# Optimization experiments

Measured on AMD Instinct MI355X. Metric: run time of the kernel, lower is better.

Reference implementation:

```python
import jax, jax.numpy as jnp
import numpy as np

B, T, N, E = 8, 64, 32, 256          # batch, seq_len, subgraph nodes, subgraph edges
D, H = 512, 8                        # embed dim, GAT heads (head dim D//H)
NV = 60000                           # total graph nodes (rows of X)
LS, LG = 10000, 60000                # last_idx_senses, last_idx_globals
V = LG - LS                          # globals vocab = 50000
DH = D // H
H1 = D                               # h1 state dim (include_senses=False)
CI = 2 * D                           # concatenated input dim


def setup_inputs() -> dict:
    key = jax.random.key(0)
    ks = jax.random.split(key, 32)
    s = 0.02
    inp = {
        "x_indices": jax.random.randint(ks[0], (B, T, N), 0, NV),
        "edge_index": jax.random.randint(ks[1], (B, T, 2, E), 0, N),
        "X": jax.random.normal(ks[2], (NV, D), jnp.float32) * s,
        "W_gat": jax.random.normal(ks[3], (D, D), jnp.float32) * s,
        "att_src": jax.random.normal(ks[4], (H, DH), jnp.float32) * s,
        "att_dst": jax.random.normal(ks[5], (H, DH), jnp.float32) * s,
        "b_gat": jnp.zeros((D,), jnp.float32),
        "Wz1": jax.random.normal(ks[6], (CI, H1), jnp.float32) * s,
        "Uz1": jax.random.normal(ks[7], (H1, H1), jnp.float32) * s,
        "Wr1": jax.random.normal(ks[8], (CI, H1), jnp.float32) * s,
        "Ur1": jax.random.normal(ks[9], (H1, H1), jnp.float32) * s,
        "W1": jax.random.normal(ks[10], (CI, H1), jnp.float32) * s,
        "bW1": jnp.zeros((H1,), jnp.float32),
        "U1": jax.random.normal(ks[11], (H1, H1), jnp.float32) * s,
        "bU1": jnp.zeros((H1,), jnp.float32),
        "Wz2": jax.random.normal(ks[12], (H1, D), jnp.float32) * s,
        "Uz2": jax.random.normal(ks[13], (D, D), jnp.float32) * s,
        "Wr2": jax.random.normal(ks[14], (H1, D), jnp.float32) * s,
        "Ur2": jax.random.normal(ks[15], (D, D), jnp.float32) * s,
        "W2": jax.random.normal(ks[16], (H1, D), jnp.float32) * s,
        "bW2": jnp.zeros((D,), jnp.float32),
        "U2": jax.random.normal(ks[17], (D, D), jnp.float32) * s,
        "bU2": jnp.zeros((D,), jnp.float32),
        "Wg": jax.random.normal(ks[18], (D, V), jnp.float32) * s,
        "bg": jnp.zeros((V,), jnp.float32),
    }
    return inp


def _gat(x, src, dst, W_gat, att_src, att_dst, b_gat):
    # x: [N,D]; src/dst: [E+N] (self-loops appended). PyG GATConv, concat heads.
    xW = (x @ W_gat).reshape(N, H, DH)                     # [N,H,DH]
    a_s = jnp.einsum('nhd,hd->nh', xW, att_src)
    a_d = jnp.einsum('nhd,hd->nh', xW, att_dst)
    e = jax.nn.leaky_relu(a_s[src] + a_d[dst], 0.2)        # [Etot,H]
    m = jax.ops.segment_max(e, dst, num_segments=N)
    m = jnp.where(jnp.isfinite(m), m, 0.0)
    ex = jnp.exp(e - m[dst])
    den = jax.ops.segment_sum(ex, dst, num_segments=N)
    alpha = ex / (den[dst] + 1e-16)                        # softmax per target node
    out = jax.ops.segment_sum(alpha[:, :, None] * xW[src], dst, num_segments=N)
    return out.reshape(N, D) + b_gat


def reference(x_indices, edge_index, X, W_gat, att_src, att_dst, b_gat,
              Wz1, Uz1, Wr1, Ur1, W1, bW1, U1, bU1,
              Wz2, Uz2, Wr2, Ur2, W2, bW2, U2, bU2, Wg, bg):
    S = B * T
    idx = x_indices.reshape(S, N)
    ei = edge_index.reshape(S, 2, E)
    loops = jnp.broadcast_to(jnp.arange(N), (S, N))
    src = jnp.concatenate([ei[:, 0], loops], axis=1)       # [S, E+N]
    dst = jnp.concatenate([ei[:, 1], loops], axis=1)

    x_nodes = X[idx]                                       # [S,N,D] gather
    gat = jax.vmap(lambda xs, s_, d_: _gat(xs, s_, d_, W_gat, att_src, att_dst, b_gat))
    gat_out = gat(x_nodes, src, dst)                       # [S,N,D]

    # input_signals = [current word embedding, GAT state of node 0]
    inp = jnp.concatenate([x_nodes[:, 0, :], gat_out[:, 0, :]], axis=1)  # [S,2D]

    def step(carry, u):
        h1, h2 = carry
        z1 = jax.nn.sigmoid(u @ Wz1 + h1 @ Uz1)
        r1 = jax.nn.sigmoid(u @ Wr1 + h1 @ Ur1)
        ht1 = jnp.tanh(u @ W1 + bW1 + (r1 * h1) @ U1 + bU1)
        h1n = z1 * ht1 + (1.0 - z1) * h1
        z2 = jax.nn.sigmoid(h1n @ Wz2 + h2 @ Uz2)
        r2 = jax.nn.sigmoid(h1n @ Wr2 + h2 @ Ur2)
        ht2 = jnp.tanh(h1n @ W2 + bW2 + (r2 * h2) @ U2 + bU2)
        h2n = z2 * ht2 + (1.0 - z2) * h2
        # torch code overwrites memory via .data.copy_ -> recurrence is detached
        new_carry = (jax.lax.stop_gradient(h1n), jax.lax.stop_gradient(h2n))
        return new_carry, h2n

    carry0 = (jnp.zeros((H1,), inp.dtype), jnp.zeros((D,), inp.dtype))
    _, H2 = jax.lax.scan(step, carry0, inp)                # [S,D]

    logits = H2 @ Wg + bg                                  # [S,V]
    return jax.nn.log_softmax(logits, axis=-1)
```

## Files before the change

### kernel.cpp

```cpp
#include <hip/hip_runtime.h>


typedef unsigned short u16;
typedef unsigned long long u64;
typedef __attribute__((ext_vector_type(8))) short s16x8;
typedef __attribute__((ext_vector_type(8))) u16  u16x8;
typedef __attribute__((ext_vector_type(4))) float f32x4;

__device__ __forceinline__ float bf2f(u16 u) {
    unsigned int x = ((unsigned int)u) << 16;
    return __uint_as_float(x);
}
__device__ __forceinline__ u16 f2bf(float f) {
    unsigned int x = __float_as_uint(f);
    x = x + 0x7fffu + ((x >> 16) & 1u);
    return (u16)(x >> 16);
}
__device__ __forceinline__ float sigmoidf_(float x) { return 1.f / (1.f + __expf(-x)); }
__device__ __forceinline__ float ldin(const void* p, size_t i, int m) {
    return m ? ((const float*)p)[i] : bf2f(((const u16*)p)[i]);
}
__device__ __forceinline__ bool nanf_(float v) { return !(v == v); }

__device__ __forceinline__ u64 packtag(float v, unsigned int e) {
    return ((u64)e << 32) | (u64)__float_as_uint(v);
}
__device__ __forceinline__ float tagval(u64 x) { return __uint_as_float((unsigned int)x); }
__device__ __forceinline__ unsigned int tagof(u64 x) { return (unsigned int)(x >> 32); }

#define AL64(p) __hip_atomic_load((p), __ATOMIC_RELAXED, __HIP_MEMORY_SCOPE_AGENT)
#define AS64(p, v) __hip_atomic_store((p), (v), __ATOMIC_RELAXED, __HIP_MEMORY_SCOPE_AGENT)

#define S_SEQ 512
#define NND   32
#define DIM   512
#define NHEAD 8
#define CI    1024
#define NV3   1536
#define VOC   50000
#define KWG   64
#define TSTEPS 512

#define OFF_MODE    0
#define OFF_FLAGS   4
#define OFF_ROWSUM  256
#define OFF_G1      4096
#define OFF_G2      12288
#define OFF_R1      20480
#define OFF_R2      24576
#define ZERO_BYTES  28672
#define OFF_WAS     28672
#define OFF_WAD     45056
#define OFF_INP     61440
#define OFF_A1      1110016
#define OFF_H2      4255744
#define OFF_WST     4780032
#define OFF_WCATT   9498624
#define OFF_WGT     12644352
#define WGT_BYTES   (50048ull * 512ull * 2ull)
#define WS_NEED_BIG (12644352ull + WGT_BYTES)

__global__ void detect_mode(const void* X, int* mode) {
    const u16* p = (const u16*)X;
    int tid = threadIdx.x;
    int hits = 0;
    for (int i = tid; i < 1024; i += 64) {
        u16 u = p[i];
        if ((u & 0x7f80u) >= 0x4000u) hits++;
    }
    hits += __shfl_xor(hits, 1);  hits += __shfl_xor(hits, 2);
    hits += __shfl_xor(hits, 4);  hits += __shfl_xor(hits, 8);
    hits += __shfl_xor(hits, 16); hits += __shfl_xor(hits, 32);
    if (tid == 0) *mode = (hits > 8) ? 1 : 0;
}

__global__ void prep_att(const void* __restrict__ Wgat, const void* __restrict__ asrc,
                         const void* __restrict__ adst, float* __restrict__ WAs,
                         float* __restrict__ WAd, const int* __restrict__ modep) {
    const int m = *modep;
    int id = blockIdx.x * 256 + threadIdx.x;
    int which = id >> 12;
    int rem = id & 4095;
    int d = rem >> 3, h = rem & 7;
    const void* att = which ? adst : asrc;
    float sum = 0.f;
#pragma unroll 8
    for (int k = 0; k < 64; ++k)
        sum += ldin(Wgat, d * 512 + h * 64 + k, m) * ldin(att, h * 64 + k, m);
    (which ? WAd : WAs)[d * 8 + h] = sum;
}

struct Ptrs9 { const void* p[9]; };
__global__ void transpose9(Ptrs9 ps, u16* __restrict__ dst, const int* __restrict__ modep) {
    const int m = *modep;
    __shared__ u16 tile[32][33];
    const void* src = ps.p[blockIdx.z];
    u16* d = dst + (size_t)blockIdx.z * 262144;
    int c0 = blockIdx.x * 32, r0 = blockIdx.y * 32;
    int tx = threadIdx.x & 31, ty = threadIdx.x >> 5;
#pragma unroll
    for (int i = 0; i < 32; i += 8)
        tile[ty + i][tx] = f2bf(ldin(src, (size_t)(r0 + ty + i) * 512 + c0 + tx, m));
    __syncthreads();
#pragma unroll
    for (int i = 0; i < 32; i += 8)
        d[(size_t)(c0 + ty + i) * 512 + r0 + tx] = tile[tx][ty + i];
}

struct Ptrs3 { const void* p[3]; };
__global__ void transpose3(Ptrs3 ps, u16* __restrict__ dst, const int* __restrict__ modep) {
    const int m = *modep;
    __shared__ u16 tile[32][33];
    const void* src = ps.p[blockIdx.z];
    u16* d = dst + (size_t)blockIdx.z * 524288;
    int c0 = blockIdx.x * 32, r0 = blockIdx.y * 32;
    int tx = threadIdx.x & 31, ty = threadIdx.x >> 5;
#pragma unroll
    for (int i = 0; i < 32; i += 8)
        tile[ty + i][tx] = f2bf(ldin(src, (size_t)(r0 + ty + i) * 512 + c0 + tx, m));
    __syncthreads();
#pragma unroll
    for (int i = 0; i < 32; i += 8)
        d[(size_t)(c0 + ty + i) * 1024 + r0 + tx] = tile[tx][ty + i];
}

__global__ void transpose_wg(const void* __restrict__ Wg, u16* __restrict__ dst,
                             const int* __restrict__ modep) {
    const int m = *modep;
    __shared__ u16 tile[32][33];
    int c0 = blockIdx.x * 32;
    int r0 = blockIdx.y * 32;
    int tx = threadIdx.x & 31, ty = threadIdx.x >> 5;
#pragma unroll
    for (int i = 0; i < 32; i += 8) {
        int n = c0 + tx;
        tile[ty + i][tx] = (n < VOC)
            ? f2bf(ldin(Wg, (size_t)(r0 + ty + i) * VOC + n, m)) : (u16)0;
    }
    __syncthreads();
#pragma unroll
    for (int i = 0; i < 32; i += 8) {
        int n = c0 + ty + i;
        if (n < VOC) dst[(size_t)n * 512 + r0 + tx] = tile[tx][ty + i];
    }
}

__global__ __launch_bounds__(256) void gat_kernel(
    const int* __restrict__ xidx, const int* __restrict__ eidx,
    const void* __restrict__ X, const void* __restrict__ Wgat,
    const float* __restrict__ WAs, const float* __restrict__ WAd,
    const void* __restrict__ bgat, u16* __restrict__ inp,
    const int* __restrict__ modep, int* __restrict__ flags) {
    const int m = *modep;
    int s = blockIdx.x, tid = threadIdx.x;
    __shared__ int idxL[NND];
    __shared__ int srcL[260];
    __shared__ int nsrcL;
    __shared__ float asL[NND][NHEAD];
    __shared__ float ad0[NHEAD];
    __shared__ float scoresL[257 * NHEAD];
    __shared__ float denL[NHEAD];
    __shared__ float xbL[NHEAD][DIM];

    if (tid < NND) idxL[tid] = xidx[s * NND + tid];
    if (tid == 0) nsrcL = 0;
    __syncthreads();

    {
        int n = tid >> 3, h = tid & 7;
        size_t xoff = (size_t)idxL[n] * DIM;
        float acc = 0.f, accd = 0.f;
        for (int d = 0; d < DIM; ++d) {
            float xv = ldin(X, xoff + d, m);
            acc  += xv * WAs[d * 8 + h];
            accd += xv * WAd[d * 8 + h];
        }
        asL[n][h] = acc;
        if (n == 0) ad0[h] = accd;
    }
    {
        int dstn = eidx[s * 512 + 256 + tid];
        if (dstn == 0) {
            int p = atomicAdd(&nsrcL, 1);
            srcL[p] = eidx[s * 512 + tid];
        }
        if (tid == 0) { int p = atomicAdd(&nsrcL, 1); srcL[p] = 0; }
    }
    __syncthreads();
    int nsrc = nsrcL;

    for (int p = tid; p < nsrc * NHEAD; p += 256) {
        int le = p >> 3, h = p & 7;
        float e = asL[srcL[le]][h] + ad0[h];
        e = (e >= 0.f) ? e : 0.2f * e;
        scoresL[le * 8 + h] = e;
    }
    __syncthreads();
    if (tid < NHEAD) {
        int h = tid;
        float mx = -1e30f;
        for (int le = 0; le < nsrc; ++le) mx = fmaxf(mx, scoresL[le * 8 + h]);
        float den = 0.f;
        for (int le = 0; le < nsrc; ++le) {
            float ex = __expf(scoresL[le * 8 + h] - mx);
            scoresL[le * 8 + h] = ex;
            den += ex;
        }
        denL[h] = den + 1e-16f;
    }
    __syncthreads();
    for (int p = tid; p < NHEAD * DIM; p += 256) {
        int d = p & 511, h = p >> 9;
        float acc = 0.f;
        for (int le = 0; le < nsrc; ++le)
            acc += scoresL[le * 8 + h] * ldin(X, (size_t)idxL[srcL[le]] * DIM + d, m);
        xbL[h][d] = acc / denL[h];
    }
    __syncthreads();
    for (int c = tid; c < DIM; c += 256) {
        int h = c >> 6;
        float acc = 0.f;
        for (int d = 0; d < DIM; ++d)
            acc += xbL[h][d] * ldin(Wgat, d * 512 + c, m);
        acc += ldin(bgat, c, m);
        float xv = ldin(X, (size_t)idxL[0] * DIM + c, m);
        if (nanf_(acc)) { atomicOr(flags, 1); acc = 0.f; }
        if (nanf_(xv))  { atomicOr(flags, 1); xv  = 0.f; }
        inp[(size_t)s * CI + DIM + c] = f2bf(acc);
        inp[(size_t)s * CI + c] = f2bf(xv);
    }
}

__global__ __launch_bounds__(256) void gemm_a1(
    const u16* __restrict__ A, const u16* __restrict__ BT,
    const void* __restrict__ bW1, const void* __restrict__ bU1,
    float* __restrict__ C, const int* __restrict__ modep, int* __restrict__ flags) {
    const int m = *modep;
    const int K = CI;
    int tid = threadIdx.x, wave = tid >> 6, lane = tid & 63;
    int mw = wave & 1, nw = wave >> 1, l15 = lane & 15, q = lane >> 4;
    int mbase = blockIdx.y * 64 + mw * 32;
    int nbase = blockIdx.x * 128 + nw * 64;
    f32x4 acc[2][4];
#pragma unroll
    for (int mi = 0; mi < 2; ++mi)
#pragma unroll
        for (int ni = 0; ni < 4; ++ni) acc[mi][ni] = (f32x4){0.f, 0.f, 0.f, 0.f};
    for (int k0 = 0; k0 < K; k0 += 32) {
        s16x8 a[2], b[4];
#pragma unroll
        for (int mi = 0; mi < 2; ++mi)
            a[mi] = *(const s16x8*)(A + (size_t)(mbase + mi * 16 + l15) * K + k0 + q * 8);
#pragma unroll
        for (int ni = 0; ni < 4; ++ni)
            b[ni] = *(const s16x8*)(BT + (size_t)(nbase + ni * 16 + l15) * K + k0 + q * 8);
#pragma unroll
        for (int mi = 0; mi < 2; ++mi)
#pragma unroll
            for (int ni = 0; ni < 4; ++ni)
                acc[mi][ni] = __builtin_amdgcn_mfma_f32_16x16x32_bf16(a[mi], b[ni], acc[mi][ni], 0, 0, 0);
    }
#pragma unroll
    for (int mi = 0; mi < 2; ++mi)
#pragma unroll
        for (int r = 0; r < 4; ++r) {
            int row = mbase + mi * 16 + q * 4 + r;
#pragma unroll
            for (int ni = 0; ni < 4; ++ni) {
                int col = nbase + ni * 16 + l15;
                float v = acc[mi][ni][r];
                if (col >= 1024) v += ldin(bW1, col - 1024, m) + ldin(bU1, col - 1024, m);
                if (nanf_(v)) { atomicOr(flags, 2); v = 0.f; }
                C[(size_t)row * NV3 + col] = v;
            }
        }
}

__global__ __launch_bounds__(256) void scan_kernel(
    const float* __restrict__ A1, const u16* __restrict__ wsT,
    const void* __restrict__ bW2, const void* __restrict__ bU2,
    u64* __restrict__ h1x, u64* __restrict__ h2x,
    u64* __restrict__ r1x, u64* __restrict__ r2x,
    u16* __restrict__ H2,
    const int* __restrict__ modep, int* __restrict__ flags) {
    const int m_ = *modep;
    const int wg = blockIdx.x;
    const int tid = threadIdx.x;
    const int jj = tid & 7, g = tid >> 3;
    const int j0 = wg * 8;
    const int lane = tid & 63, wave = tid >> 6;

    __shared__ float h1c[512], h2c[512], r1c[512], r2c[512];
    __shared__ float red[4][7][8];

    u16x8 wreg[14];
#pragma unroll
    for (int m = 0; m < 7; ++m) {
        const u16* src = wsT + (size_t)m * 262144 + (size_t)(j0 + jj) * 512 + g * 16;
        wreg[2 * m]     = *(const u16x8*)src;
        wreg[2 * m + 1] = *(const u16x8*)(src + 8);
    }
    const u16* u1col = wsT + (size_t)7 * 262144 + (size_t)(j0 + jj) * 512;
    const u16* u2col = wsT + (size_t)8 * 262144 + (size_t)(j0 + jj) * 512;
    const u16x8 u1w0 = *(const u16x8*)(u1col + g * 16);
    const u16x8 u1w1 = *(const u16x8*)(u1col + g * 16 + 8);
    const u16x8 u2w0 = *(const u16x8*)(u2col + g * 16);
    const u16x8 u2w1 = *(const u16x8*)(u2col + g * 16 + 8);
    const float bsum = (tid < 8) ? (ldin(bW2, j0 + tid, m_) + ldin(bU2, j0 + tid, m_)) : 0.f;

    for (int t = 0; t <= TSTEPS; ++t) {
        const bool need1 = (t < TSTEPS), need2 = (t >= 1);
        float azv = 0.f, arv = 0.f, awk = 0.f;
        if (tid < 8 && need1) {
            const float* a1p = A1 + (size_t)t * NV3 + j0 + tid;
            azv = a1p[0]; arv = a1p[512]; awk = a1p[1024];
        }
        {
            const unsigned int eg1 = (unsigned int)t;
            const unsigned int eg2 = (t >= 2) ? (unsigned int)t : 0u;
            u64* p1 = h1x + (size_t)(t & 1) * 512 + 2 * tid;
            u64* p2 = h2x + (size_t)((t + 1) & 1) * 512 + 2 * tid;
            u64 x0, x1, y0, y1;
            for (;;) {
                x0 = AL64(p1); x1 = AL64(p1 + 1);
                y0 = AL64(p2); y1 = AL64(p2 + 1);
                if (tagof(x0) == eg1 && tagof(x1) == eg1 &&
                    tagof(y0) == eg2 && tagof(y1) == eg2) break;
                __builtin_amdgcn_s_sleep(1);
            }
            h1c[2 * tid] = tagval(x0); h1c[2 * tid + 1] = tagval(x1);
            h2c[2 * tid] = tagval(y0); h2c[2 * tid + 1] = tagval(y1);
        }
        __syncthreads();
        {
            float q1 = 0.f, q3 = 0.f, q6 = 0.f;
#pragma unroll
            for (int u = 0; u < 8; ++u) {
                const int k = g * 16 + u;
                const float x1 = h1c[k], x2 = h2c[k];
                q1 = fmaf(x1, bf2f(wreg[2 * 1][u]), q1);
                q3 = fmaf(x1, bf2f(wreg[2 * 3][u]), q3);
                q6 = fmaf(x2, bf2f(wreg[2 * 6][u]), q6);
            }
#pragma unroll
            for (int u = 0; u < 8; ++u) {
                const int k = g * 16 + 8 + u;
                const float x1 = h1c[k], x2 = h2c[k];
                q1 = fmaf(x1, bf2f(wreg[2 * 1 + 1][u]), q1);
                q3 = fmaf(x1, bf2f(wreg[2 * 3 + 1][u]), q3);
                q6 = fmaf(x2, bf2f(wreg[2 * 6 + 1][u]), q6);
            }
            q1 += __shfl_xor(q1, 8); q1 += __shfl_xor(q1, 16); q1 += __shfl_xor(q1, 32);
            q3 += __shfl_xor(q3, 8); q3 += __shfl_xor(q3, 16); q3 += __shfl_xor(q3, 32);
            q6 += __shfl_xor(q6, 8); q6 += __shfl_xor(q6, 16); q6 += __shfl_xor(q6, 32);
            if (lane < 8) {
                red[wave][0][lane] = q1;
                red[wave][1][lane] = q3;
                red[wave][2][lane] = q6;
            }
        }
        __syncthreads();
        if (tid < 8) {
            float s1 = red[0][0][tid] + red[1][0][tid] + red[2][0][tid] + red[3][0][tid];
            float s3 = red[0][1][tid] + red[1][1][tid] + red[2][1][tid] + red[3][1][tid];
            float s6 = red[0][2][tid] + red[1][2][tid] + red[2][2][tid] + red[3][2][tid];
            int j = j0 + tid;
            if (need1) AS64(&r1x[j], packtag(sigmoidf_(arv + s1), (unsigned int)t));
            if (need2) AS64(&r2x[j], packtag(sigmoidf_(s3 + s6), (unsigned int)t));
        }
        {
            float q0 = 0.f, q2 = 0.f, q4 = 0.f, q5 = 0.f;
#pragma unroll
            for (int u = 0; u < 8; ++u) {
                const int k = g * 16 + u;
                const float x1 = h1c[k], x2 = h2c[k];
                q0 = fmaf(x1, bf2f(wreg[2 * 0][u]), q0);
                q2 = fmaf(x1, bf2f(wreg[2 * 2][u]), q2);
                q4 = fmaf(x1, bf2f(wreg[2 * 4][u]), q4);
                q5 = fmaf(x2, bf2f(wreg[2 * 5][u]), q5);
            }
#pragma unroll
            for (int u = 0; u < 8; ++u) {
                const int k = g * 16 + 8 + u;
                const float x1 = h1c[k], x2 = h2c[k];
                q0 = fmaf(x1, bf2f(wreg[2 * 0 + 1][u]), q0);
                q2 = fmaf(x1, bf2f(wreg[2 * 2 + 1][u]), q2);
                q4 = fmaf(x1, bf2f(wreg[2 * 4 + 1][u]), q4);
                q5 = fmaf(x2, bf2f(wreg[2 * 5 + 1][u]), q5);
            }
            q0 += __shfl_xor(q0, 8); q0 += __shfl_xor(q0, 16); q0 += __shfl_xor(q0, 32);
            q2 += __shfl_xor(q2, 8); q2 += __shfl_xor(q2, 16); q2 += __shfl_xor(q2, 32);
            q4 += __shfl_xor(q4, 8); q4 += __shfl_xor(q4, 16); q4 += __shfl_xor(q4, 32);
            q5 += __shfl_xor(q5, 8); q5 += __shfl_xor(q5, 16); q5 += __shfl_xor(q5, 32);
            if (lane < 8) {
                red[wave][3][lane] = q0;
                red[wave][4][lane] = q2;
                red[wave][5][lane] = q4;
                red[wave][6][lane] = q5;
            }
        }
        {
            u64 a0 = 0, a1 = 0, b0 = 0, b1 = 0;
            u64* q1p = r1x + 2 * tid;
            u64* q2p = r2x + 2 * tid;
            const unsigned int er = (unsigned int)t;
            for (;;) {
                if (need1) { a0 = AL64(q1p); a1 = AL64(q1p + 1); }
                if (need2) { b0 = AL64(q2p); b1 = AL64(q2p + 1); }
                bool ok = true;
                if (need1) ok = ok && (tagof(a0) == er) && (tagof(a1) == er);
                if (need2) ok = ok && (tagof(b0) == er) && (tagof(b1) == er);
                if (ok) break;
                __builtin_amdgcn_s_sleep(1);
            }
            if (need1) { r1c[2 * tid] = tagval(a0); r1c[2 * tid + 1] = tagval(a1); }
            if (need2) { r2c[2 * tid] = tagval(b0); r2c[2 * tid + 1] = tagval(b1); }
        }
        __syncthreads();
        {
            float pa = 0.f, pb = 0.f;
#pragma unroll
            for (int u = 0; u < 8; ++u) {
                const int k = g * 16 + u;
                pa = fmaf(r1c[k] * h1c[k], bf2f(u1w0[u]), pa);
                pb = fmaf(r2c[k] * h2c[k], bf2f(u2w0[u]), pb);
            }
#pragma unroll
            for (int u = 0; u < 8; ++u) {
                const int k = g * 16 + 8 + u;
                pa = fmaf(r1c[k] * h1c[k], bf2f(u1w1[u]), pa);
                pb = fmaf(r2c[k] * h2c[k], bf2f(u2w1[u]), pb);
            }
            pa += __shfl_xor(pa, 8); pa += __shfl_xor(pa, 16); pa += __shfl_xor(pa, 32);
            pb += __shfl_xor(pb, 8); pb += __shfl_xor(pb, 16); pb += __shfl_xor(pb, 32);
            if (lane < 8) {
                red[wave][0][lane] = pa;
                red[wave][1][lane] = pb;
            }
        }
        __syncthreads();
        if (tid < 8) {
            float spa = red[0][0][tid] + red[1][0][tid] + red[2][0][tid] + red[3][0][tid];
            float spb = red[0][1][tid] + red[1][1][tid] + red[2][1][tid] + red[3][1][tid];
            float s0  = red[0][3][tid] + red[1][3][tid] + red[2][3][tid] + red[3][3][tid];
            float s2  = red[0][4][tid] + red[1][4][tid] + red[2][4][tid] + red[3][4][tid];
            float s4  = red[0][5][tid] + red[1][5][tid] + red[2][5][tid] + red[3][5][tid];
            float s5  = red[0][6][tid] + red[1][6][tid] + red[2][6][tid] + red[3][6][tid];
            int j = j0 + tid;
            if (need1) {
                float z1 = sigmoidf_(azv + s0);
                float ht1 = tanhf(awk + spa);
                float g1n = z1 * ht1 + (1.f - z1) * h1c[j];
                if (nanf_(g1n)) { atomicOr(flags, 4); g1n = 0.f; }
                AS64(&h1x[(size_t)((t + 1) & 1) * 512 + j], packtag(g1n, (unsigned int)(t + 1)));
            }
            if (need2) {
                float z2 = sigmoidf_(s2 + s5);
                float ht2 = tanhf(s4 + bsum + spb);
                float g2n = z2 * ht2 + (1.f - z2) * h2c[j];
                if (nanf_(g2n)) { atomicOr(flags, 4); g2n = 0.f; }
                AS64(&h2x[(size_t)(t & 1) * 512 + j], packtag(g2n, (unsigned int)(t + 1)));
                H2[(size_t)(t - 1) * 512 + j] = f2bf(g2n);
            }
        }
        __syncthreads();
    }
}

__global__ __launch_bounds__(256) void gemm_logits_fast(
    const u16* __restrict__ H2, const u16* __restrict__ WgT,
    const void* __restrict__ bg, void* __restrict__ out,
    float* __restrict__ rowsum, const int* __restrict__ modep, int* __restrict__ flags) {
    const int m = *modep;
    const int K = DIM;
    int tid = threadIdx.x, wave = tid >> 6, lane = tid & 63;
    int mw = wave & 1, nw = wave >> 1, l15 = lane & 15, q = lane >> 4;
    int mbase = blockIdx.y * 64 + mw * 32;
    int nbase = blockIdx.x * 128 + nw * 64;
    f32x4 acc[2][4];
#pragma unroll
    for (int mi = 0; mi < 2; ++mi)
#pragma unroll
        for (int ni = 0; ni < 4; ++ni) acc[mi][ni] = (f32x4){0.f, 0.f, 0.f, 0.f};
    for (int k0 = 0; k0 < K; k0 += 32) {
        s16x8 a[2], b[4];
#pragma unroll
        for (int mi = 0; mi < 2; ++mi)
            a[mi] = *(const s16x8*)(H2 + (size_t)(mbase + mi * 16 + l15) * K + k0 + q * 8);
#pragma unroll
        for (int ni = 0; ni < 4; ++ni) {
            int n = nbase + ni * 16 + l15;
            if (n >= VOC) n = VOC - 1;
            b[ni] = *(const s16x8*)(WgT + (size_t)n * 512 + k0 + q * 8);
        }
#pragma unroll
        for (int mi = 0; mi < 2; ++mi)
#pragma unroll
            for (int ni = 0; ni < 4; ++ni)
                acc[mi][ni] = __builtin_amdgcn_mfma_f32_16x16x32_bf16(a[mi], b[ni], acc[mi][ni], 0, 0, 0);
    }
    __shared__ float lds_rows[64];
    if (tid < 64) lds_rows[tid] = 0.f;
    __syncthreads();
#pragma unroll
    for (int mi = 0; mi < 2; ++mi)
#pragma unroll
        for (int r = 0; r < 4; ++r) {
            int row = mbase + mi * 16 + q * 4 + r;
            float esum = 0.f;
#pragma unroll
            for (int ni = 0; ni < 4; ++ni) {
                int col = nbase + ni * 16 + l15;
                float v = acc[mi][ni][r];
                if (col < VOC) {
                    v += ldin(bg, col, m);
                    if (nanf_(v)) { atomicOr(flags, 8); v = 0.f; }
                    if (m) ((float*)out)[(size_t)row * VOC + col] = v;
                    else   ((u16*)out)[(size_t)row * VOC + col] = f2bf(v);
                    esum += __expf(v);
                }
            }
            esum += __shfl_xor(esum, 1); esum += __shfl_xor(esum, 2);
            esum += __shfl_xor(esum, 4); esum += __shfl_xor(esum, 8);
            if (l15 == 0) atomicAdd(&lds_rows[row - blockIdx.y * 64], esum);
        }
    __syncthreads();
    if (tid < 64) atomicAdd(&rowsum[blockIdx.y * 64 + tid], lds_rows[tid]);
}

__global__ __launch_bounds__(256) void gemm_logits_slow(
    const u16* __restrict__ H2, const void* __restrict__ Wg,
    const void* __restrict__ bg, void* __restrict__ out,
    float* __restrict__ rowsum, const int* __restrict__ modep, int* __restrict__ flags) {
    const int m = *modep;
    const int K = DIM;
    int tid = threadIdx.x, wave = tid >> 6, lane = tid & 63;
    int mw = wave & 1, nw = wave >> 1, l15 = lane & 15, q = lane >> 4;
    int mbase = blockIdx.y * 64 + mw * 32;
    int nbase = blockIdx.x * 128 + nw * 64;
    f32x4 acc[2][4];
#pragma unroll
    for (int mi = 0; mi < 2; ++mi)
#pragma unroll
        for (int ni = 0; ni < 4; ++ni) acc[mi][ni] = (f32x4){0.f, 0.f, 0.f, 0.f};
    for (int k0 = 0; k0 < K; k0 += 32) {
        s16x8 a[2], b[4];
#pragma unroll
        for (int mi = 0; mi < 2; ++mi)
            a[mi] = *(const s16x8*)(H2 + (size_t)(mbase + mi * 16 + l15) * K + k0 + q * 8);
#pragma unroll
        for (int ni = 0; ni < 4; ++ni) {
            int n = nbase + ni * 16 + l15;
            if (n >= VOC) n = VOC - 1;
            size_t kb = (size_t)(k0 + q * 8) * VOC + n;
#pragma unroll
            for (int j = 0; j < 8; ++j) b[ni][j] = (short)f2bf(ldin(Wg, kb + (size_t)j * VOC, m));
        }
#pragma unroll
        for (int mi = 0; mi < 2; ++mi)
#pragma unroll
            for (int ni = 0; ni < 4; ++ni)
                acc[mi][ni] = __builtin_amdgcn_mfma_f32_16x16x32_bf16(a[mi], b[ni], acc[mi][ni], 0, 0, 0);
    }
    __shared__ float lds_rows[64];
    if (tid < 64) lds_rows[tid] = 0.f;
    __syncthreads();
#pragma unroll
    for (int mi = 0; mi < 2; ++mi)
#pragma unroll
        for (int r = 0; r < 4; ++r) {
            int row = mbase + mi * 16 + q * 4 + r;
            float esum = 0.f;
#pragma unroll
            for (int ni = 0; ni < 4; ++ni) {
                int col = nbase + ni * 16 + l15;
                float v = acc[mi][ni][r];
                if (col < VOC) {
                    v += ldin(bg, col, m);
                    if (nanf_(v)) { atomicOr(flags, 8); v = 0.f; }
                    if (m) ((float*)out)[(size_t)row * VOC + col] = v;
                    else   ((u16*)out)[(size_t)row * VOC + col] = f2bf(v);
                    esum += __expf(v);
                }
            }
            esum += __shfl_xor(esum, 1); esum += __shfl_xor(esum, 2);
            esum += __shfl_xor(esum, 4); esum += __shfl_xor(esum, 8);
            if (l15 == 0) atomicAdd(&lds_rows[row - blockIdx.y * 64], esum);
        }
    __syncthreads();
    if (tid < 64) atomicAdd(&rowsum[blockIdx.y * 64 + tid], lds_rows[tid]);
}

__global__ __launch_bounds__(256) void logsoftmax_fix(void* __restrict__ out,
                                                      const float* __restrict__ rowsum,
                                                      const int* __restrict__ modep,
                                                      int* __restrict__ flags) {
    const int m = *modep;
    int row = blockIdx.y;
    int c0 = blockIdx.x * 2048 + threadIdx.x * 8;
    if (c0 >= VOC) return;
    float rs = rowsum[row];
    float ls = logf(rs);
    if (nanf_(ls) || !(rs > 0.f)) { atomicOr(flags, 16); ls = 0.f; }
    float sentinel = 0.f;
    if (row == 0 && c0 == 0) {
        int f = *flags;
        if (f) sentinel = 1000.f * (float)__ffs(f);
    }
    size_t base = (size_t)row * VOC + c0;
    if (m) {
        float* o = (float*)out;
        int lim = (c0 + 8 <= VOC) ? 8 : (VOC - c0);
        for (int i = 0; i < lim; ++i) {
            float v = o[base + i] - ls;
            if (i == 0) v += sentinel;
            o[base + i] = v;
        }
    } else {
        u16* o = (u16*)out;
        int lim = (c0 + 8 <= VOC) ? 8 : (VOC - c0);
        for (int i = 0; i < lim; ++i) {
            float v = bf2f(o[base + i]) - ls;
            if (i == 0) v += sentinel;
            o[base + i] = f2bf(v);
        }
    }
}

extern "C" void kernel_launch(void* const* d_in, const int* in_sizes, int n_in,
                              void* d_out, int out_size, void* d_ws, size_t ws_size,
                              hipStream_t stream) {
    const int* xidx = (const int*)d_in[0];
    const int* eidx = (const int*)d_in[1];
    const void* X    = d_in[2];
    const void* Wgat = d_in[3];
    const void* asrc = d_in[4];
    const void* adst = d_in[5];
    const void* bgat = d_in[6];
    const void* Wz1  = d_in[7];
    const void* Uz1  = d_in[8];
    const void* Wr1  = d_in[9];
    const void* Ur1  = d_in[10];
    const void* W1   = d_in[11];
    const void* bW1  = d_in[12];
    const void* U1   = d_in[13];
    const void* bU1  = d_in[14];
    const void* Wz2  = d_in[15];
    const void* Uz2  = d_in[16];
    const void* Wr2  = d_in[17];
    const void* Ur2  = d_in[18];
    const void* W2   = d_in[19];
    const void* bW2  = d_in[20];
    const void* U2   = d_in[21];
    const void* bU2  = d_in[22];
    const void* Wg   = d_in[23];
    const void* bg   = d_in[24];

    char* ws = (char*)d_ws;
    int*   modep  = (int*)(ws + OFF_MODE);
    int*   flags  = (int*)(ws + OFF_FLAGS);
    float* rowsum = (float*)(ws + OFF_ROWSUM);
    u64*   h1x    = (u64*)(ws + OFF_G1);
    u64*   h2x    = (u64*)(ws + OFF_G2);
    u64*   r1x    = (u64*)(ws + OFF_R1);
    u64*   r2x    = (u64*)(ws + OFF_R2);
    float* WAs    = (float*)(ws + OFF_WAS);
    float* WAd    = (float*)(ws + OFF_WAD);
    u16*   inp    = (u16*)(ws + OFF_INP);
    float* A1     = (float*)(ws + OFF_A1);
    u16*   H2     = (u16*)(ws + OFF_H2);
    u16*   wsT    = (u16*)(ws + OFF_WST);
    u16*   WcatT  = (u16*)(ws + OFF_WCATT);
    u16*   WgT    = (u16*)(ws + OFF_WGT);

    const bool big = ws_size >= WS_NEED_BIG;

    (void)hipMemsetAsync(ws, 0, ZERO_BYTES, stream);

    detect_mode<<<1, 64, 0, stream>>>(X, modep);

    prep_att<<<32, 256, 0, stream>>>(Wgat, asrc, adst, WAs, WAd, modep);

    Ptrs9 p9;
    p9.p[0] = Uz1; p9.p[1] = Ur1; p9.p[2] = Wz2; p9.p[3] = Wr2; p9.p[4] = W2;
    p9.p[5] = Uz2; p9.p[6] = Ur2; p9.p[7] = U1;  p9.p[8] = U2;
    transpose9<<<dim3(16, 16, 9), 256, 0, stream>>>(p9, wsT, modep);

    Ptrs3 p3; p3.p[0] = Wz1; p3.p[1] = Wr1; p3.p[2] = W1;
    transpose3<<<dim3(16, 32, 3), 256, 0, stream>>>(p3, WcatT, modep);

    if (big)
        transpose_wg<<<dim3((VOC + 31) / 32, 16), 256, 0, stream>>>(Wg, WgT, modep);

    gat_kernel<<<S_SEQ, 256, 0, stream>>>(xidx, eidx, X, Wgat, WAs, WAd, bgat, inp, modep, flags);

    gemm_a1<<<dim3(NV3 / 128, S_SEQ / 64), 256, 0, stream>>>(inp, WcatT, bW1, bU1, A1, modep, flags);

    scan_kernel<<<KWG, 256, 0, stream>>>(A1, wsT, bW2, bU2, h1x, h2x, r1x, r2x, H2, modep, flags);

    if (big)
        gemm_logits_fast<<<dim3((VOC + 127) / 128, S_SEQ / 64), 256, 0, stream>>>(H2, WgT, bg, d_out, rowsum, modep, flags);
    else
        gemm_logits_slow<<<dim3((VOC + 127) / 128, S_SEQ / 64), 256, 0, stream>>>(H2, Wg, bg, d_out, rowsum, modep, flags);

    logsoftmax_fix<<<dim3(25, S_SEQ), 256, 0, stream>>>(d_out, rowsum, modep, flags);
}
```

Before: 2.609 ms.

## Read r-gates directly into registers per group and split gate finalization across threads

Each thread group now polls the 16 tagged r1/r2 values it needs straight into registers, dropping the shared r1c/r2c staging and one block-wide barrier per step. The r1/r2 and h1/h2 finalization work is split across threads 0-7 and 8-15 so the two layers' gates run in parallel. tanhf is replaced with an exp-based fast tanh. In exchange, each thread issues more global atomic loads when polling, which adds redundant traffic, and the fast tanh loses some accuracy for large inputs.

```diff
diff --git a/kernel.cpp b/kernel.cpp
--- a/kernel.cpp
+++ b/kernel.cpp
@@ -17,6 +17,9 @@
     return (u16)(x >> 16);
 }
 __device__ __forceinline__ float sigmoidf_(float x) { return 1.f / (1.f + __expf(-x)); }
+__device__ __forceinline__ float tanhfast_(float x) {
+    return 1.f - 2.f / (__expf(2.f * x) + 1.f);
+}
 __device__ __forceinline__ float ldin(const void* p, size_t i, int m) {
     return m ? ((const float*)p)[i] : bf2f(((const u16*)p)[i]);
 }
@@ -290,8 +293,8 @@
     const int j0 = wg * 8;
     const int lane = tid & 63, wave = tid >> 6;
 
-    __shared__ float h1c[512], h2c[512], r1c[512], r2c[512];
-    __shared__ float red[4][7][8];
+    __shared__ float h1c[512], h2c[512];
+    __shared__ float red[4][9][8];
 
     u16x8 wreg[14];
 #pragma unroll
@@ -306,7 +309,8 @@
     const u16x8 u1w1 = *(const u16x8*)(u1col + g * 16 + 8);
     const u16x8 u2w0 = *(const u16x8*)(u2col + g * 16);
     const u16x8 u2w1 = *(const u16x8*)(u2col + g * 16 + 8);
-    const float bsum = (tid < 8) ? (ldin(bW2, j0 + tid, m_) + ldin(bU2, j0 + tid, m_)) : 0.f;
+    const float bsum = (tid >= 8 && tid < 16)
+        ? (ldin(bW2, j0 + tid - 8, m_) + ldin(bU2, j0 + tid - 8, m_)) : 0.f;
 
     for (int t = 0; t <= TSTEPS; ++t) {
         const bool need1 = (t < TSTEPS), need2 = (t >= 1);
@@ -361,12 +365,17 @@
         }
         __syncthreads();
         if (tid < 8) {
-            float s1 = red[0][0][tid] + red[1][0][tid] + red[2][0][tid] + red[3][0][tid];
-            float s3 = red[0][1][tid] + red[1][1][tid] + red[2][1][tid] + red[3][1][tid];
-            float s6 = red[0][2][tid] + red[1][2][tid] + red[2][2][tid] + red[3][2][tid];
-            int j = j0 + tid;
-            if (need1) AS64(&r1x[j], packtag(sigmoidf_(arv + s1), (unsigned int)t));
-            if (need2) AS64(&r2x[j], packtag(sigmoidf_(s3 + s6), (unsigned int)t));
+            if (need1) {
+                float s1 = red[0][0][tid] + red[1][0][tid] + red[2][0][tid] + red[3][0][tid];
+                AS64(&r1x[j0 + tid], packtag(sigmoidf_(arv + s1), (unsigned int)t));
+            }
+        } else if (tid < 16) {
+            if (need2) {
+                int l = tid - 8;
+                float s3 = red[0][1][l] + red[1][1][l] + red[2][1][l] + red[3][1][l];
+                float s6 = red[0][2][l] + red[1][2][l] + red[2][2][l] + red[3][2][l];
+                AS64(&r2x[j0 + l], packtag(sigmoidf_(s3 + s6), (unsigned int)t));
+            }
         }
         {
             float q0 = 0.f, q2 = 0.f, q4 = 0.f, q5 = 0.f;
@@ -399,64 +408,85 @@
                 red[wave][6][lane] = q5;
             }
         }
+        float r1f[16], r2f[16];
         {
-            u64 a0 = 0, a1 = 0, b0 = 0, b1 = 0;
-            u64* q1p = r1x + 2 * tid;
-            u64* q2p = r2x + 2 * tid;
             const unsigned int er = (unsigned int)t;
-            for (;;) {
-                if (need1) { a0 = AL64(q1p); a1 = AL64(q1p + 1); }
-                if (need2) { b0 = AL64(q2p); b1 = AL64(q2p + 1); }
-                bool ok = true;
-                if (need1) ok = ok && (tagof(a0) == er) && (tagof(a1) == er);
-                if (need2) ok = ok && (tagof(b0) == er) && (tagof(b1) == er);
-                if (ok) break;
-                __builtin_amdgcn_s_sleep(1);
-            }
-            if (need1) { r1c[2 * tid] = tagval(a0); r1c[2 * tid + 1] = tagval(a1); }
-            if (need2) { r2c[2 * tid] = tagval(b0); r2c[2 * tid + 1] = tagval(b1); }
-        }
-        __syncthreads();
+            u64 a[16];
+            if (need1) {
+                for (;;) {
+                    bool ok = true;
+#pragma unroll
+                    for (int u = 0; u < 16; ++u) a[u] = AL64(&r1x[g * 16 + u]);
+#pragma unroll
+                    for (int u = 0; u < 16; ++u) ok = ok && (tagof(a[u]) == er);
+                    if (ok) break;
+                    __builtin_amdgcn_s_sleep(1);
+                }
+#pragma unroll
+                for (int u = 0; u < 16; ++u) r1f[u] = tagval(a[u]);
+            } else {
+#pragma unroll
+                for (int u = 0; u < 16; ++u) r1f[u] = 0.f;
+            }
+            if (need2) {
+                for (;;) {
+                    bool ok = true;
+#pragma unroll
+                    for (int u = 0; u < 16; ++u) a[u] = AL64(&r2x[g * 16 + u]);
+#pragma unroll
+                    for (int u = 0; u < 16; ++u) ok = ok && (tagof(a[u]) == er);
+                    if (ok) break;
+                    __builtin_amdgcn_s_sleep(1);
+                }
+#pragma unroll
+                for (int u = 0; u < 16; ++u) r2f[u] = tagval(a[u]);
+            } else {
+#pragma unroll
+                for (int u = 0; u < 16; ++u) r2f[u] = 0.f;
+            }
+        }
         {
             float pa = 0.f, pb = 0.f;
 #pragma unroll
             for (int u = 0; u < 8; ++u) {
                 const int k = g * 16 + u;
-                pa = fmaf(r1c[k] * h1c[k], bf2f(u1w0[u]), pa);
-                pb = fmaf(r2c[k] * h2c[k], bf2f(u2w0[u]), pb);
+                pa = fmaf(r1f[u] * h1c[k], bf2f(u1w0[u]), pa);
+                pb = fmaf(r2f[u] * h2c[k], bf2f(u2w0[u]), pb);
             }
 #pragma unroll
             for (int u = 0; u < 8; ++u) {
                 const int k = g * 16 + 8 + u;
-                pa = fmaf(r1c[k] * h1c[k], bf2f(u1w1[u]), pa);
-                pb = fmaf(r2c[k] * h2c[k], bf2f(u2w1[u]), pb);
+                pa = fmaf(r1f[8 + u] * h1c[k], bf2f(u1w1[u]), pa);
+                pb = fmaf(r2f[8 + u] * h2c[k], bf2f(u2w1[u]), pb);
             }
             pa += __shfl_xor(pa, 8); pa += __shfl_xor(pa, 16); pa += __shfl_xor(pa, 32);
             pb += __shfl_xor(pb, 8); pb += __shfl_xor(pb, 16); pb += __shfl_xor(pb, 32);
             if (lane < 8) {
-                red[wave][0][lane] = pa;
-                red[wave][1][lane] = pb;
+                red[wave][7][lane] = pa;
+                red[wave][8][lane] = pb;
             }
         }
         __syncthreads();
         if (tid < 8) {
-            float spa = red[0][0][tid] + red[1][0][tid] + red[2][0][tid] + red[3][0][tid];
-            float spb = red[0][1][tid] + red[1][1][tid] + red[2][1][tid] + red[3][1][tid];
-            float s0  = red[0][3][tid] + red[1][3][tid] + red[2][3][tid] + red[3][3][tid];
-            float s2  = red[0][4][tid] + red[1][4][tid] + red[2][4][tid] + red[3][4][tid];
-            float s4  = red[0][5][tid] + red[1][5][tid] + red[2][5][tid] + red[3][5][tid];
-            float s5  = red[0][6][tid] + red[1][6][tid] + red[2][6][tid] + red[3][6][tid];
-            int j = j0 + tid;
             if (need1) {
+                float spa = red[0][7][tid] + red[1][7][tid] + red[2][7][tid] + red[3][7][tid];
+                float s0  = red[0][3][tid] + red[1][3][tid] + red[2][3][tid] + red[3][3][tid];
+                int j = j0 + tid;
                 float z1 = sigmoidf_(azv + s0);
-                float ht1 = tanhf(awk + spa);
+                float ht1 = tanhfast_(awk + spa);
                 float g1n = z1 * ht1 + (1.f - z1) * h1c[j];
                 if (nanf_(g1n)) { atomicOr(flags, 4); g1n = 0.f; }
                 AS64(&h1x[(size_t)((t + 1) & 1) * 512 + j], packtag(g1n, (unsigned int)(t + 1)));
             }
+        } else if (tid < 16) {
             if (need2) {
+                int l = tid - 8, j = j0 + l;
+                float spb = red[0][8][l] + red[1][8][l] + red[2][8][l] + red[3][8][l];
+                float s2  = red[0][4][l] + red[1][4][l] + red[2][4][l] + red[3][4][l];
+                float s4  = red[0][5][l] + red[1][5][l] + red[2][5][l] + red[3][5][l];
+                float s5  = red[0][6][l] + red[1][6][l] + red[2][6][l] + red[3][6][l];
                 float z2 = sigmoidf_(s2 + s5);
-                float ht2 = tanhf(s4 + bsum + spb);
+                float ht2 = tanhfast_(s4 + bsum + spb);
                 float g2n = z2 * ht2 + (1.f - z2) * h2c[j];
                 if (nanf_(g2n)) { atomicOr(flags, 4); g2n = 0.f; }
                 AS64(&h2x[(size_t)(t & 1) * 512 + j], packtag(g2n, (unsigned int)(t + 1)));
```

New measurement: 3.053 ms. +17.0%, slower.
